# Kernel optimization log

Hardware: AMD Instinct MI355X
Metric: run time of the kernel (lower is better)

The kernel has to match this reference:

```python
import jax, jax.numpy as jnp
import numpy as np

N = 256
DT = 1.0 / 4096.0
BATCH = 256
LENGTH = 4096

def _legt_transition(n):
    # HiPPO-LegT continuous-time transition (Gu et al.)
    Q = np.arange(n, dtype=np.float64)
    R = (2.0 * Q + 1.0) ** 0.5
    j, i = np.meshgrid(Q, Q)
    A = R[:, None] * np.where(i < j, (-1.0) ** (i - j), 1.0) * R[None, :]
    B = R[:, None]
    return -A, B

def _bilinear(A, B, dt):
    # scipy cont2discrete(method='bilinear'), alpha=0.5
    n = A.shape[0]
    ima = np.eye(n) - 0.5 * dt * A
    Ad = np.linalg.solve(ima, np.eye(n) + 0.5 * dt * A)
    Bd = np.linalg.solve(ima, dt * B)
    return Ad, Bd

def setup_inputs() -> dict:
    key = jax.random.key(0)
    Ac, Bc = _legt_transition(N)
    evals = (2.0 * np.arange(N, dtype=np.float64) + 1.0) ** 0.5
    C = evals @ Ac                        # (N,) readout from continuous A
    D = np.sum(evals * Bc.squeeze(-1))    # scalar
    scale = 1.0 / (1.0 - 0.5 * D * DT)
    C_discr = (scale * 0.5 * DT * C).astype(np.float32)          # (N,)
    D_discr = np.array([scale * (1.0 + 0.5 * DT * D)], np.float32)  # (1,)
    Ad, Bd = _bilinear(Ac, Bc, DT)
    inputs = jax.random.normal(key, (BATCH, LENGTH), dtype=jnp.float32)
    return {
        "inputs": inputs,
        "A": jnp.asarray(Ad, dtype=jnp.float32),
        "B": jnp.asarray(Bd.squeeze(-1), dtype=jnp.float32),
        "C_discr": jnp.asarray(C_discr),
        "D_discr": jnp.asarray(D_discr),
    }

def reference(inputs, A, B, C_discr, D_discr):
    # inputs: (batch, length). teacher_ratio=1.0 -> fully teacher-forced LTI scan:
    #   c_t = A c_{t-1} + B * u_t ;  pred_t = fac_t * (c_t @ C) + D * u_t
    # where fac_0 = 1 and fac_t = 2 for t > 0 (as in the torch loop).
    batch, length = inputs.shape
    c0 = jnp.zeros((batch, A.shape[0]), dtype=inputs.dtype)
    facs = jnp.where(jnp.arange(length) == 0, 1.0, 2.0).astype(inputs.dtype)

    def step(c, xs):
        x_t, fac = xs                                   # x_t: (batch,)
        c = c @ A.T + B[None, :] * x_t[:, None]         # (batch, N); F.linear(c, A)
        pred = fac * (c @ C_discr) + D_discr[0] * x_t   # (batch,)
        return c, pred

    _, preds = jax.lax.scan(step, c0, (inputs.T, facs))  # preds: (length, batch)
    return preds.T  # (batch, length)
```

## Files before the change

### kernel.cpp

```cpp
#include <hip/hip_runtime.h>


#define LENGTH 4096

#define WS_P2    0
#define WS_P4    65536
#define WS_P8    131072
#define WS_P16   196608
#define WS_P32   262144
#define WS_P64T  327680
#define WS_P128T 393216
#define WS_W     458752
#define WS_V     475136
#define WS_XH    491520
#define WS_XL    1015808
#define WS_AH    1540096
#define WS_AL    1605632

typedef __attribute__((ext_vector_type(8))) short bf16x8;
typedef __attribute__((ext_vector_type(4))) float f32x4;
#define MFMA(a, b, c) __builtin_amdgcn_mfma_f32_16x16x32_bf16(a, b, c, 0, 0, 0)

__device__ inline unsigned short f2bf(float f) {
    unsigned int u = __float_as_uint(f);
    return (unsigned short)((u + 0x7FFFu + ((u >> 16) & 1u)) >> 16);
}
__device__ inline void split2(float f, short& h, short& l) {
    unsigned short hu = f2bf(f);
    float fh = __uint_as_float((unsigned int)hu << 16);
    h = (short)hu;
    l = (short)f2bf(f - fh);
}

__device__ __forceinline__ void mm_body(const float* __restrict__ X,
                                        const float* __restrict__ Y,
                                        float* __restrict__ Z,
                                        int row, int t, bool trans, float* red) {
    const int j = t & 255, p = t >> 8;
    const float* xr = X + row * 256 + 64 * p;
    const float* yc = Y + (64 * p) * 256 + j;
    float a0 = 0.f, a1 = 0.f, a2 = 0.f, a3 = 0.f;
#pragma unroll
    for (int l = 0; l < 64; l += 4) {
        a0 = fmaf(xr[l + 0], yc[(l + 0) * 256], a0);
        a1 = fmaf(xr[l + 1], yc[(l + 1) * 256], a1);
        a2 = fmaf(xr[l + 2], yc[(l + 2) * 256], a2);
        a3 = fmaf(xr[l + 3], yc[(l + 3) * 256], a3);
    }
    float s = (a0 + a1) + (a2 + a3);
    if (p) red[(p - 1) * 256 + j] = s;
    __syncthreads();
    if (!p) {
        float z = s + red[j] + red[256 + j] + red[512 + j];
        if (trans) Z[j * 256 + row] = z;
        else       Z[row * 256 + j] = z;
    }
}

__global__ __launch_bounds__(1024) void fused0(const float* __restrict__ A,
                                               const float* __restrict__ x,
                                               float* __restrict__ P2,
                                               short* __restrict__ XH,
                                               short* __restrict__ XL) {
    __shared__ float red[3 * 256];
    const int t = threadIdx.x;
    if (blockIdx.x < 256) {
        mm_body(A, A, P2, blockIdx.x, t, false, red);
        return;
    }
    const int wv = t >> 6, lane = t & 63;
    const int pj = (blockIdx.x - 256) * 16 + wv;
    const int c = pj >> 4, blk = pj & 15;
    const int b = blk * 16 + (lane & 15);
    const int s0 = c * 32 + 8 * (lane >> 4);
    const float4 v0 = reinterpret_cast<const float4*>(&x[b * LENGTH + s0])[0];
    const float4 v1 = reinterpret_cast<const float4*>(&x[b * LENGTH + s0])[1];
    const float f[8] = {v0.x, v0.y, v0.z, v0.w, v1.x, v1.y, v1.z, v1.w};
    bf16x8 hv, lv;
#pragma unroll
    for (int e = 0; e < 8; ++e) {
        short h, l;
        split2(f[e], h, l);
        hv[e] = h; lv[e] = l;
    }
    const int off = (pj * 64 + lane) * 8;
    *reinterpret_cast<bf16x8*>(XH + off) = hv;
    *reinterpret_cast<bf16x8*>(XL + off) = lv;
}

__global__ __launch_bounds__(1024) void mmsq(const float* __restrict__ S,
                                             float* __restrict__ D) {
    __shared__ float red[3 * 256];
    mm_body(S, S, D, blockIdx.x, threadIdx.x, false, red);
}
__global__ __launch_bounds__(1024) void mmsqT(const float* __restrict__ S,
                                              float* __restrict__ D) {
    __shared__ float red[3 * 256];
    mm_body(S, S, D, blockIdx.x, threadIdx.x, true, red);
}

__global__ __launch_bounds__(1024) void p128w(const float* __restrict__ P64T,
                                              float* __restrict__ P128T,
                                              const float* __restrict__ A,
                                              const float* __restrict__ C,
                                              const float* __restrict__ P16,
                                              const float* __restrict__ P32,
                                              float* __restrict__ W) {
    __shared__ float red[3 * 256];
    __shared__ float cur[256];
    __shared__ float red4[4][256];
    const int t = threadIdx.x;
    if (blockIdx.x < 256) {
        mm_body(P64T, P64T, P128T, blockIdx.x, t, false, red);
        return;
    }
    const int c = blockIdx.x - 256;
    const int j = t & 255, p = t >> 8;
    float areg[64];
#pragma unroll
    for (int ii = 0; ii < 64; ++ii) areg[ii] = A[(64 * p + ii) * 256 + j];

    if (c == 0) {
        if (t < 256) cur[t] = C[t];
        __syncthreads();
    } else {
        const float* M1 = (c == 2) ? P32 : P16;
        float s0 = 0.f, s1 = 0.f;
#pragma unroll
        for (int ii = 0; ii < 64; ii += 2) {
            s0 = fmaf(C[64 * p + ii],     M1[(64 * p + ii) * 256 + j],     s0);
            s1 = fmaf(C[64 * p + ii + 1], M1[(64 * p + ii + 1) * 256 + j], s1);
        }
        red4[p][j] = s0 + s1;
        __syncthreads();
        if (!p) cur[j] = red4[0][j] + red4[1][j] + red4[2][j] + red4[3][j];
        __syncthreads();
        if (c == 3) {
            float q0 = 0.f, q1 = 0.f;
#pragma unroll
            for (int ii = 0; ii < 64; ii += 2) {
                q0 = fmaf(cur[64 * p + ii],     P32[(64 * p + ii) * 256 + j],     q0);
                q1 = fmaf(cur[64 * p + ii + 1], P32[(64 * p + ii + 1) * 256 + j], q1);
            }
            red4[p][j] = q0 + q1;
            __syncthreads();
            if (!p) cur[j] = red4[0][j] + red4[1][j] + red4[2][j] + red4[3][j];
            __syncthreads();
        }
    }
    for (int s_ = 0; s_ < 16; ++s_) {
        if (!p) W[(16 * c + s_) * 256 + j] = cur[j];
        if (s_ == 15) break;
        float s0 = 0.f, s1 = 0.f;
#pragma unroll
        for (int m = 0; m < 16; ++m) {
            float4 c4 = *reinterpret_cast<const float4*>(&cur[64 * p + 4 * m]);
            s0 = fmaf(c4.x, areg[4 * m + 0], s0);
            s1 = fmaf(c4.y, areg[4 * m + 1], s1);
            s0 = fmaf(c4.z, areg[4 * m + 2], s0);
            s1 = fmaf(c4.w, areg[4 * m + 3], s1);
        }
        red4[p][j] = s0 + s1;
        __syncthreads();
        if (!p) cur[j] = red4[0][j] + red4[1][j] + red4[2][j] + red4[3][j];
        __syncthreads();
    }
}

__global__ __launch_bounds__(1024) void vgen(const float* __restrict__ P64T,
                                             const float* __restrict__ P128T,
                                             const float* __restrict__ B,
                                             float* __restrict__ V) {
    __shared__ float cur[256];
    __shared__ float red4[4][256];
    const int t = threadIdx.x;
    const int i = t & 255, p = t >> 8;
    const int c = blockIdx.x;
    float mreg[64];
#pragma unroll
    for (int jj = 0; jj < 64; ++jj) mreg[jj] = P128T[(64 * p + jj) * 256 + i];

    if (c == 0) {
        if (t < 256) cur[t] = B[t];
        __syncthreads();
    } else {
        float s0 = 0.f, s1 = 0.f;
#pragma unroll
        for (int jj = 0; jj < 64; jj += 2) {
            s0 = fmaf(P64T[(64 * p + jj) * 256 + i],     B[64 * p + jj],     s0);
            s1 = fmaf(P64T[(64 * p + jj + 1) * 256 + i], B[64 * p + jj + 1], s1);
        }
        red4[p][i] = s0 + s1;
        __syncthreads();
        if (!p) cur[i] = red4[0][i] + red4[1][i] + red4[2][i] + red4[3][i];
        __syncthreads();
    }
    for (int s_ = 0; s_ < 32; ++s_) {
        if (!p) V[(2 * s_ + c) * 256 + i] = cur[i];
        if (s_ == 31) break;
        float s0 = 0.f, s1 = 0.f;
#pragma unroll
        for (int m = 0; m < 16; ++m) {
            float4 c4 = *reinterpret_cast<const float4*>(&cur[64 * p + 4 * m]);
            s0 = fmaf(c4.x, mreg[4 * m + 0], s0);
            s1 = fmaf(c4.y, mreg[4 * m + 1], s1);
            s0 = fmaf(c4.z, mreg[4 * m + 2], s0);
            s1 = fmaf(c4.w, mreg[4 * m + 3], s1);
        }
        red4[p][i] = s0 + s1;
        __syncthreads();
        if (!p) cur[i] = red4[0][i] + red4[1][i] + red4[2][i] + red4[3][i];
        __syncthreads();
    }
}

__global__ __launch_bounds__(256) void kfrag(const float* __restrict__ Wm,
                                             const float* __restrict__ Vm,
                                             short* __restrict__ AH,
                                             short* __restrict__ AL) {
    const int bid = blockIdx.x, t = threadIdx.x;
    __shared__ float Wl[64 * 257];
    __shared__ float Vl[3 * 256];
    __shared__ float kl[144];
    for (int r = 0; r < 64; ++r) Wl[r * 257 + t] = Wm[r * 256 + t];
#pragma unroll
    for (int qq = 0; qq < 3; ++qq) {
        const int q = 2 * bid - 1 + qq;
        Vl[qq * 256 + t] = (q >= 0) ? Vm[q * 256 + t] : 0.f;
    }
    __syncthreads();
    if (t < 143) {
        const int tau = 128 * bid - 15 + t;
        float s = 0.f;
        if (tau >= 0) {
            const int r = tau & 63;
            const int qq = (tau >> 6) - (2 * bid - 1);
            const float* wr = &Wl[r * 257];
            const float* vr = &Vl[qq * 256];
            float s0 = 0.f, s1 = 0.f, s2 = 0.f, s3 = 0.f;
#pragma unroll 16
            for (int i = 0; i < 256; i += 4) {
                s0 = fmaf(wr[i + 0], vr[i + 0], s0);
                s1 = fmaf(wr[i + 1], vr[i + 1], s1);
                s2 = fmaf(wr[i + 2], vr[i + 2], s2);
                s3 = fmaf(wr[i + 3], vr[i + 3], s3);
            }
            s = (s0 + s1) + (s2 + s3);
        }
        kl[t] = s;
    }
    __syncthreads();
    const int wv = t >> 6, lane = t & 63;
#pragma unroll
    for (int e2 = 0; e2 < 2; ++e2) {
        const int ep = 2 * wv + e2;
        const int m = 8 * bid + ep;
        bf16x8 hv, lv;
#pragma unroll
        for (int el = 0; el < 8; ++el) {
            const int rel = 16 * ep + (lane & 15) - 8 * (lane >> 4) - el + 15;
            short h, l;
            split2(kl[rel], h, l);
            hv[el] = h; lv[el] = l;
        }
        const int off = (m * 64 + lane) * 8;
        *reinterpret_cast<bf16x8*>(AH + off) = hv;
        *reinterpret_cast<bf16x8*>(AL + off) = lv;
    }
}

#define AHP(M_) (*reinterpret_cast<const bf16x8*>(AH + ((M_) * 64 + lane) * 8))
#define ALP(M_) (*reinterpret_cast<const bf16x8*>(AL + ((M_) * 64 + lane) * 8))
#define XHP(O_) (*reinterpret_cast<const bf16x8*>(XH + (O_)))
#define XLP(O_) (*reinterpret_cast<const bf16x8*>(XL + (O_)))

#define ONER6(AHF, ALF, T, R)                                   \
    acc[T][R][0] = MFMA(AHF, bh0, acc[T][R][0]);                \
    acc[T][R][1] = MFMA(AHF, bh1, acc[T][R][1]);                \
    acc[T][R][0] = MFMA(AHF, bl0, acc[T][R][0]);                \
    acc[T][R][1] = MFMA(AHF, bl1, acc[T][R][1]);                \
    acc[T][R][0] = MFMA(ALF, bh0, acc[T][R][0]);                \
    acc[T][R][1] = MFMA(ALF, bh1, acc[T][R][1]);

#define APPLYT(T)                                               \
    { if (d >= 0)      { ONER6(ah0, al0, T, 0) }                \
      if (d + 16 >= 0) { ONER6(ah1, al1, T, 1) }                \
      if (d + 32 >= 0) { ONER6(ah2, al2, T, 2) }                \
      if (d + 48 >= 0) { ONER6(ah3, al3, T, 3) } }

#define LOADA_FULL(D_)                                          \
    { const int m0_ = ((D_) > 0 ? (D_) : 0) >> 4;               \
      const int m1_ = ((D_) + 16 > 0 ? (D_) + 16 : 0) >> 4;     \
      const int m2_ = ((D_) + 32 > 0 ? (D_) + 32 : 0) >> 4;     \
      const int m3_ = ((D_) + 48 > 0 ? (D_) + 48 : 0) >> 4;     \
      ah0 = AHP(m0_); al0 = ALP(m0_);                           \
      ah1 = AHP(m1_); al1 = ALP(m1_);                           \
      ah2 = AHP(m2_); al2 = ALP(m2_);                           \
      ah3 = AHP(m3_); al3 = ALP(m3_); }

__global__ __launch_bounds__(512) void convm(const short* __restrict__ XH,
                                             const short* __restrict__ XL,
                                             const short* __restrict__ AH,
                                             const short* __restrict__ AL,
                                             const float* __restrict__ x,
                                             const float* __restrict__ Dp,
                                             float* __restrict__ out) {
    const int pr = blockIdx.x & 31;
    const int bt = blockIdx.x >> 5;
    const int tid = threadIdx.x;
    const int w = tid >> 6, lane = tid & 63;
    const int tA64 = pr * 64, tB64 = (63 - pr) * 64;
    const int nA = 2 * pr + 2;
    const int bt2 = bt * 2;
    __shared__ float lds[16 * 64 * 34];

    f32x4 acc[2][4][2];
#pragma unroll
    for (int t_ = 0; t_ < 2; ++t_)
#pragma unroll
        for (int r_ = 0; r_ < 4; ++r_)
#pragma unroll
            for (int c_ = 0; c_ < 2; ++c_) acc[t_][r_][c_] = f32x4{0.f, 0.f, 0.f, 0.f};

    const int lo = (130 * w) >> 3, hi = (130 * (w + 1)) >> 3;

    bf16x8 ah0, ah1, ah2, ah3, al0, al1, al2, al3, bh0, bh1, bl0, bl1;
    int idx = lo;
    int tile = (idx < nA) ? 0 : 1;
    int cc = idx - (tile ? nA : 0);
    int d = (tile ? tB64 : tA64) - 32 * cc;
    LOADA_FULL(d);
    {
        const int xo = ((cc * 16 + bt2) * 64 + lane) * 8;
        bh0 = XHP(xo); bh1 = XHP(xo + 512);
        bl0 = XLP(xo); bl1 = XLP(xo + 512);
    }

    while (true) {
        const int nxt = idx + 1;
        const bool hn = nxt < hi;
        bf16x8 tbh0, tbh1, tbl0, tbl1, tah0, tah1, tal0, tal1;
        int tilen = tile, dn = d;
        bool sw = false;
        if (hn) {
            tilen = (nxt < nA) ? 0 : 1;
            const int ccn = nxt - (tilen ? nA : 0);
            dn = (tilen ? tB64 : tA64) - 32 * ccn;
            sw = (tilen != tile);
            const int xo = ((ccn * 16 + bt2) * 64 + lane) * 8;
            tbh0 = XHP(xo); tbh1 = XHP(xo + 512);
            tbl0 = XLP(xo); tbl1 = XLP(xo + 512);
            if (!sw) {
                const int n0 = (dn > 0 ? dn : 0) >> 4;
                const int n1 = (dn + 16 > 0 ? dn + 16 : 0) >> 4;
                tah0 = AHP(n0); tal0 = ALP(n0);
                tah1 = AHP(n1); tal1 = ALP(n1);
            }
        }
        if (tile == 0) { APPLYT(0) } else { APPLYT(1) }
        if (!hn) break;
        if (!sw) {
            ah3 = ah1; ah2 = ah0; al3 = al1; al2 = al0;
            ah0 = tah0; ah1 = tah1; al0 = tal0; al1 = tal1;
        } else {
            LOADA_FULL(dn);
        }
        bh0 = tbh0; bh1 = tbh1; bl0 = tbl0; bl1 = tbl1;
        tile = tilen; d = dn; idx = nxt;
    }

    const int lq = lane >> 4, lr = lane & 15;
#pragma unroll
    for (int t_ = 0; t_ < 2; ++t_)
#pragma unroll
        for (int r_ = 0; r_ < 4; ++r_)
#pragma unroll
            for (int c_ = 0; c_ < 2; ++c_)
#pragma unroll
                for (int e_ = 0; e_ < 4; ++e_)
                    lds[((w * 2 + t_) * 64 + (r_ * 16 + lq * 4 + e_)) * 34 +
                        (c_ * 16 + lr)] = acc[t_][r_][c_][e_];
    __syncthreads();

    const float D = Dp[0];
    const int b = tid >> 4;
    const int t4 = (tid & 15) * 4;
#pragma unroll
    for (int t_ = 0; t_ < 2; ++t_) {
        const int tbase = t_ ? tB64 : tA64;
        float s0 = 0.f, s1 = 0.f, s2 = 0.f, s3 = 0.f;
#pragma unroll
        for (int w_ = 0; w_ < 8; ++w_) {
            const float* lp = &lds[((w_ * 2 + t_) * 64 + t4) * 34 + b];
            s0 += lp[0]; s1 += lp[34]; s2 += lp[68]; s3 += lp[102];
        }
        const int g = (bt * 32 + b) * LENGTH + tbase + t4;
        const float4 xv = *reinterpret_cast<const float4*>(x + g);
        float4 o;
        o.x = 2.f * s0 + D * xv.x;
        o.y = 2.f * s1 + D * xv.y;
        o.z = 2.f * s2 + D * xv.z;
        o.w = 2.f * s3 + D * xv.w;
        if (tbase == 0 && t4 == 0) o.x -= s0;
        *reinterpret_cast<float4*>(out + g) = o;
    }
}

extern "C" void kernel_launch(void* const* d_in, const int* in_sizes, int n_in,
                              void* d_out, int out_size, void* d_ws, size_t ws_size,
                              hipStream_t stream) {
    const float* x  = (const float*)d_in[0];
    const float* A  = (const float*)d_in[1];
    const float* B  = (const float*)d_in[2];
    const float* C  = (const float*)d_in[3];
    const float* Dp = (const float*)d_in[4];
    float* out = (float*)d_out;
    float* ws  = (float*)d_ws;

    float* P2    = ws + WS_P2;
    float* P4    = ws + WS_P4;
    float* P8    = ws + WS_P8;
    float* P16   = ws + WS_P16;
    float* P32   = ws + WS_P32;
    float* P64T  = ws + WS_P64T;
    float* P128T = ws + WS_P128T;
    float* Wm    = ws + WS_W;
    float* Vm    = ws + WS_V;
    short* XHs   = (short*)(ws + WS_XH);
    short* XLs   = (short*)(ws + WS_XL);
    short* AHs   = (short*)(ws + WS_AH);
    short* ALs   = (short*)(ws + WS_AL);

    fused0<<<384, 1024, 0, stream>>>(A, x, P2, XHs, XLs);
    mmsq<<<256, 1024, 0, stream>>>(P2, P4);
    mmsq<<<256, 1024, 0, stream>>>(P4, P8);
    mmsq<<<256, 1024, 0, stream>>>(P8, P16);
    mmsq<<<256, 1024, 0, stream>>>(P16, P32);
    mmsqT<<<256, 1024, 0, stream>>>(P32, P64T);
    p128w<<<260, 1024, 0, stream>>>(P64T, P128T, A, C, P16, P32, Wm);
    vgen<<<2, 1024, 0, stream>>>(P64T, P128T, B, Vm);
    kfrag<<<32, 256, 0, stream>>>(Wm, Vm, AHs, ALs);
    convm<<<256, 512, 0, stream>>>(XHs, XLs, AHs, ALs, x, Dp, out);
}
```

Baseline: 126.4 us.

## Rebalance precompute kernels and double-buffer fragment loads in convolution kernel

Moves the W-vector generation earlier so it runs alongside the P64 squaring instead of the P128 squaring, and reorders fused0's block roles. kfrag now uses 512 threads, with each wave producing one fragment, so the kernel-fragment generation is spread across more parallelism. convm replaces its contiguous per-wave chunk walk, which shifted A fragments between tiles, with a strided (stride 8) two-frag double-buffered loop that fully reloads A and X fragments each iteration. This aims to overlap loads with MFMA work and to shorten the serial precompute chain, at the cost of more global loads per step and higher register pressure.

After: 120.5 us. 1.05x faster.

```diff
diff --git a/kernel.cpp b/kernel.cpp
--- a/kernel.cpp
+++ b/kernel.cpp
@@ -64,12 +64,12 @@
                                                short* __restrict__ XL) {
     __shared__ float red[3 * 256];
     const int t = threadIdx.x;
-    if (blockIdx.x < 256) {
-        mm_body(A, A, P2, blockIdx.x, t, false, red);
+    if (blockIdx.x >= 128) {
+        mm_body(A, A, P2, blockIdx.x - 128, t, false, red);
         return;
     }
     const int wv = t >> 6, lane = t & 63;
-    const int pj = (blockIdx.x - 256) * 16 + wv;
+    const int pj = blockIdx.x * 16 + wv;
     const int c = pj >> 4, blk = pj & 15;
     const int b = blk * 16 + (lane & 15);
     const int s0 = c * 32 + 8 * (lane >> 4);
@@ -93,28 +93,38 @@
     __shared__ float red[3 * 256];
     mm_body(S, S, D, blockIdx.x, threadIdx.x, false, red);
 }
-__global__ __launch_bounds__(1024) void mmsqT(const float* __restrict__ S,
-                                              float* __restrict__ D) {
-    __shared__ float red[3 * 256];
-    mm_body(S, S, D, blockIdx.x, threadIdx.x, true, red);
-}
-
-__global__ __launch_bounds__(1024) void p128w(const float* __restrict__ P64T,
-                                              float* __restrict__ P128T,
-                                              const float* __restrict__ A,
-                                              const float* __restrict__ C,
-                                              const float* __restrict__ P16,
-                                              const float* __restrict__ P32,
-                                              float* __restrict__ W) {
+
+__device__ __forceinline__ void rv_mm(const float* __restrict__ v,
+                                      const float* __restrict__ M,
+                                      float* curl, float (*red4)[256],
+                                      int j, int p) {
+    float s0 = 0.f, s1 = 0.f;
+#pragma unroll
+    for (int ii = 0; ii < 64; ii += 2) {
+        s0 = fmaf(v[64 * p + ii],     M[(64 * p + ii) * 256 + j],     s0);
+        s1 = fmaf(v[64 * p + ii + 1], M[(64 * p + ii + 1) * 256 + j], s1);
+    }
+    red4[p][j] = s0 + s1;
+    __syncthreads();
+    if (!p) curl[j] = red4[0][j] + red4[1][j] + red4[2][j] + red4[3][j];
+    __syncthreads();
+}
+
+__global__ __launch_bounds__(1024) void p64w(const float* __restrict__ P32,
+                                             float* __restrict__ P64T,
+                                             const float* __restrict__ A,
+                                             const float* __restrict__ C,
+                                             const float* __restrict__ P16,
+                                             float* __restrict__ W) {
     __shared__ float red[3 * 256];
     __shared__ float cur[256];
     __shared__ float red4[4][256];
     const int t = threadIdx.x;
-    if (blockIdx.x < 256) {
-        mm_body(P64T, P64T, P128T, blockIdx.x, t, false, red);
+    if (blockIdx.x >= 4) {
+        mm_body(P32, P32, P64T, blockIdx.x - 4, t, true, red);
         return;
     }
-    const int c = blockIdx.x - 256;
+    const int c = blockIdx.x;
     const int j = t & 255, p = t >> 8;
     float areg[64];
 #pragma unroll
@@ -124,29 +134,8 @@
         if (t < 256) cur[t] = C[t];
         __syncthreads();
     } else {
-        const float* M1 = (c == 2) ? P32 : P16;
-        float s0 = 0.f, s1 = 0.f;
-#pragma unroll
-        for (int ii = 0; ii < 64; ii += 2) {
-            s0 = fmaf(C[64 * p + ii],     M1[(64 * p + ii) * 256 + j],     s0);
-            s1 = fmaf(C[64 * p + ii + 1], M1[(64 * p + ii + 1) * 256 + j], s1);
-        }
-        red4[p][j] = s0 + s1;
-        __syncthreads();
-        if (!p) cur[j] = red4[0][j] + red4[1][j] + red4[2][j] + red4[3][j];
-        __syncthreads();
-        if (c == 3) {
-            float q0 = 0.f, q1 = 0.f;
-#pragma unroll
-            for (int ii = 0; ii < 64; ii += 2) {
-                q0 = fmaf(cur[64 * p + ii],     P32[(64 * p + ii) * 256 + j],     q0);
-                q1 = fmaf(cur[64 * p + ii + 1], P32[(64 * p + ii + 1) * 256 + j], q1);
-            }
-            red4[p][j] = q0 + q1;
-            __syncthreads();
-            if (!p) cur[j] = red4[0][j] + red4[1][j] + red4[2][j] + red4[3][j];
-            __syncthreads();
-        }
+        rv_mm(C, (c == 2) ? P32 : P16, cur, red4, j, p);
+        if (c == 3) rv_mm(cur, P32, cur, red4, j, p);
     }
     for (int s_ = 0; s_ < 16; ++s_) {
         if (!p) W[(16 * c + s_) * 256 + j] = cur[j];
@@ -214,23 +203,23 @@
     }
 }
 
-__global__ __launch_bounds__(256) void kfrag(const float* __restrict__ Wm,
+__global__ __launch_bounds__(512) void kfrag(const float* __restrict__ Wm,
                                              const float* __restrict__ Vm,
                                              short* __restrict__ AH,
                                              short* __restrict__ AL) {
     const int bid = blockIdx.x, t = threadIdx.x;
     __shared__ float Wl[64 * 257];
-    __shared__ float Vl[3 * 256];
-    __shared__ float kl[144];
-    for (int r = 0; r < 64; ++r) Wl[r * 257 + t] = Wm[r * 256 + t];
-#pragma unroll
-    for (int qq = 0; qq < 3; ++qq) {
-        const int q = 2 * bid - 1 + qq;
-        Vl[qq * 256 + t] = (q >= 0) ? Vm[q * 256 + t] : 0.f;
-    }
-    __syncthreads();
-    if (t < 143) {
-        const int tau = 128 * bid - 15 + t;
+    __shared__ float Vl[768];
+    __shared__ float kl[160];
+    for (int u = t; u < 16384; u += 512)
+        Wl[(u >> 8) * 257 + (u & 255)] = Wm[u];
+    for (int u = t; u < 768; u += 512) {
+        const int q = 2 * bid - 1 + (u >> 8);
+        Vl[u] = (q >= 0) ? Vm[q * 256 + (u & 255)] : 0.f;
+    }
+    __syncthreads();
+    if (t < 159) {
+        const int tau = 128 * bid - 31 + t;
         float s = 0.f;
         if (tau >= 0) {
             const int r = tau & 63;
@@ -238,12 +227,12 @@
             const float* wr = &Wl[r * 257];
             const float* vr = &Vl[qq * 256];
             float s0 = 0.f, s1 = 0.f, s2 = 0.f, s3 = 0.f;
-#pragma unroll 16
-            for (int i = 0; i < 256; i += 4) {
-                s0 = fmaf(wr[i + 0], vr[i + 0], s0);
-                s1 = fmaf(wr[i + 1], vr[i + 1], s1);
-                s2 = fmaf(wr[i + 2], vr[i + 2], s2);
-                s3 = fmaf(wr[i + 3], vr[i + 3], s3);
+#pragma unroll 8
+            for (int i2 = 0; i2 < 256; i2 += 4) {
+                s0 = fmaf(wr[i2 + 0], vr[i2 + 0], s0);
+                s1 = fmaf(wr[i2 + 1], vr[i2 + 1], s1);
+                s2 = fmaf(wr[i2 + 2], vr[i2 + 2], s2);
+                s3 = fmaf(wr[i2 + 3], vr[i2 + 3], s3);
             }
             s = (s0 + s1) + (s2 + s3);
         }
@@ -251,52 +240,70 @@
     }
     __syncthreads();
     const int wv = t >> 6, lane = t & 63;
-#pragma unroll
-    for (int e2 = 0; e2 < 2; ++e2) {
-        const int ep = 2 * wv + e2;
-        const int m = 8 * bid + ep;
-        bf16x8 hv, lv;
-#pragma unroll
-        for (int el = 0; el < 8; ++el) {
-            const int rel = 16 * ep + (lane & 15) - 8 * (lane >> 4) - el + 15;
-            short h, l;
-            split2(kl[rel], h, l);
-            hv[el] = h; lv[el] = l;
-        }
-        const int off = (m * 64 + lane) * 8;
-        *reinterpret_cast<bf16x8*>(AH + off) = hv;
-        *reinterpret_cast<bf16x8*>(AL + off) = lv;
-    }
-}
-
-#define AHP(M_) (*reinterpret_cast<const bf16x8*>(AH + ((M_) * 64 + lane) * 8))
-#define ALP(M_) (*reinterpret_cast<const bf16x8*>(AL + ((M_) * 64 + lane) * 8))
-#define XHP(O_) (*reinterpret_cast<const bf16x8*>(XH + (O_)))
-#define XLP(O_) (*reinterpret_cast<const bf16x8*>(XL + (O_)))
-
-#define ONER6(AHF, ALF, T, R)                                   \
-    acc[T][R][0] = MFMA(AHF, bh0, acc[T][R][0]);                \
-    acc[T][R][1] = MFMA(AHF, bh1, acc[T][R][1]);                \
-    acc[T][R][0] = MFMA(AHF, bl0, acc[T][R][0]);                \
-    acc[T][R][1] = MFMA(AHF, bl1, acc[T][R][1]);                \
-    acc[T][R][0] = MFMA(ALF, bh0, acc[T][R][0]);                \
-    acc[T][R][1] = MFMA(ALF, bh1, acc[T][R][1]);
-
-#define APPLYT(T)                                               \
-    { if (d >= 0)      { ONER6(ah0, al0, T, 0) }                \
-      if (d + 16 >= 0) { ONER6(ah1, al1, T, 1) }                \
-      if (d + 32 >= 0) { ONER6(ah2, al2, T, 2) }                \
-      if (d + 48 >= 0) { ONER6(ah3, al3, T, 3) } }
-
-#define LOADA_FULL(D_)                                          \
-    { const int m0_ = ((D_) > 0 ? (D_) : 0) >> 4;               \
-      const int m1_ = ((D_) + 16 > 0 ? (D_) + 16 : 0) >> 4;     \
-      const int m2_ = ((D_) + 32 > 0 ? (D_) + 32 : 0) >> 4;     \
-      const int m3_ = ((D_) + 48 > 0 ? (D_) + 48 : 0) >> 4;     \
-      ah0 = AHP(m0_); al0 = ALP(m0_);                           \
-      ah1 = AHP(m1_); al1 = ALP(m1_);                           \
-      ah2 = AHP(m2_); al2 = ALP(m2_);                           \
-      ah3 = AHP(m3_); al3 = ALP(m3_); }
+    const int m = 8 * bid + wv;
+    bf16x8 hv, lv;
+#pragma unroll
+    for (int el = 0; el < 8; ++el) {
+        const int rel = 16 * wv + (lane & 15) - 8 * (lane >> 4) - el + 31;
+        short h_, l_;
+        split2(kl[rel], h_, l_);
+        hv[el] = h_; lv[el] = l_;
+    }
+    const int off = (m * 64 + lane) * 8;
+    *reinterpret_cast<bf16x8*>(AH + off) = hv;
+    *reinterpret_cast<bf16x8*>(AL + off) = lv;
+}
+
+struct Frag {
+    bf16x8 bh0, bh1, bl0, bl1;
+    bf16x8 ah0, ah1, ah2, ah3, al0, al1, al2, al3;
+    int d0, tile;
+};
+
+#define LOADF(F, IDX_) do {                                                    \
+        const int i_ = (IDX_);                                                 \
+        const int tl_ = (i_ < nA) ? 0 : 1;                                     \
+        const int cc_ = i_ - (tl_ ? nA : 0);                                   \
+        const int xo_ = ((cc_ * 16 + bt2) * 64 + lane) * 8;                    \
+        F.bh0 = *reinterpret_cast<const bf16x8*>(XH + xo_);                    \
+        F.bh1 = *reinterpret_cast<const bf16x8*>(XH + xo_ + 512);              \
+        F.bl0 = *reinterpret_cast<const bf16x8*>(XL + xo_);                    \
+        F.bl1 = *reinterpret_cast<const bf16x8*>(XL + xo_ + 512);              \
+        const int d_ = (tl_ ? tB64 : tA64) - cc_ * 32;                         \
+        F.d0 = d_; F.tile = tl_;                                               \
+        const int m0_ = (d_ > 0 ? d_ : 0) >> 4;                                \
+        const int m1_ = (d_ + 16 > 0 ? d_ + 16 : 0) >> 4;                      \
+        const int m2_ = (d_ + 32 > 0 ? d_ + 32 : 0) >> 4;                      \
+        const int m3_ = (d_ + 48 > 0 ? d_ + 48 : 0) >> 4;                      \
+        F.ah0 = *reinterpret_cast<const bf16x8*>(AH + (m0_ * 64 + lane) * 8);  \
+        F.al0 = *reinterpret_cast<const bf16x8*>(AL + (m0_ * 64 + lane) * 8);  \
+        F.ah1 = *reinterpret_cast<const bf16x8*>(AH + (m1_ * 64 + lane) * 8);  \
+        F.al1 = *reinterpret_cast<const bf16x8*>(AL + (m1_ * 64 + lane) * 8);  \
+        F.ah2 = *reinterpret_cast<const bf16x8*>(AH + (m2_ * 64 + lane) * 8);  \
+        F.al2 = *reinterpret_cast<const bf16x8*>(AL + (m2_ * 64 + lane) * 8);  \
+        F.ah3 = *reinterpret_cast<const bf16x8*>(AH + (m3_ * 64 + lane) * 8);  \
+        F.al3 = *reinterpret_cast<const bf16x8*>(AL + (m3_ * 64 + lane) * 8);  \
+    } while (0)
+
+#define ONER(F, T, R, AHF, ALF)                                                \
+        if (F.d0 + 16 * R >= 0) {                                              \
+            acc[T][R][0] = MFMA(F.AHF, F.bh0, acc[T][R][0]);                   \
+            acc[T][R][1] = MFMA(F.AHF, F.bh1, acc[T][R][1]);                   \
+            acc[T][R][0] = MFMA(F.AHF, F.bl0, acc[T][R][0]);                   \
+            acc[T][R][1] = MFMA(F.AHF, F.bl1, acc[T][R][1]);                   \
+            acc[T][R][0] = MFMA(F.ALF, F.bh0, acc[T][R][0]);                   \
+            acc[T][R][1] = MFMA(F.ALF, F.bh1, acc[T][R][1]);                   \
+        }
+
+#define APPLY(F) do {                                                          \
+        if (F.tile == 0) {                                                     \
+            ONER(F, 0, 0, ah0, al0) ONER(F, 0, 1, ah1, al1)                    \
+            ONER(F, 0, 2, ah2, al2) ONER(F, 0, 3, ah3, al3)                    \
+        } else {                                                               \
+            ONER(F, 1, 0, ah0, al0) ONER(F, 1, 1, ah1, al1)                    \
+            ONER(F, 1, 2, ah2, al2) ONER(F, 1, 3, ah3, al3)                    \
+        }                                                                      \
+    } while (0)
 
 __global__ __launch_bounds__(512) void convm(const short* __restrict__ XH,
                                              const short* __restrict__ XL,
@@ -312,6 +319,7 @@
     const int tA64 = pr * 64, tB64 = (63 - pr) * 64;
     const int nA = 2 * pr + 2;
     const int bt2 = bt * 2;
+
     __shared__ float lds[16 * 64 * 34];
 
     f32x4 acc[2][4][2];
@@ -322,51 +330,21 @@
 #pragma unroll
             for (int c_ = 0; c_ < 2; ++c_) acc[t_][r_][c_] = f32x4{0.f, 0.f, 0.f, 0.f};
 
-    const int lo = (130 * w) >> 3, hi = (130 * (w + 1)) >> 3;
-
-    bf16x8 ah0, ah1, ah2, ah3, al0, al1, al2, al3, bh0, bh1, bl0, bl1;
-    int idx = lo;
-    int tile = (idx < nA) ? 0 : 1;
-    int cc = idx - (tile ? nA : 0);
-    int d = (tile ? tB64 : tA64) - 32 * cc;
-    LOADA_FULL(d);
-    {
-        const int xo = ((cc * 16 + bt2) * 64 + lane) * 8;
-        bh0 = XHP(xo); bh1 = XHP(xo + 512);
-        bl0 = XLP(xo); bl1 = XLP(xo + 512);
-    }
-
+    Frag f0, f1;
+    LOADF(f0, w);
+    int idx = w;
     while (true) {
-        const int nxt = idx + 1;
-        const bool hn = nxt < hi;
-        bf16x8 tbh0, tbh1, tbl0, tbl1, tah0, tah1, tal0, tal1;
-        int tilen = tile, dn = d;
-        bool sw = false;
-        if (hn) {
-            tilen = (nxt < nA) ? 0 : 1;
-            const int ccn = nxt - (tilen ? nA : 0);
-            dn = (tilen ? tB64 : tA64) - 32 * ccn;
-            sw = (tilen != tile);
-            const int xo = ((ccn * 16 + bt2) * 64 + lane) * 8;
-            tbh0 = XHP(xo); tbh1 = XHP(xo + 512);
-            tbl0 = XLP(xo); tbl1 = XLP(xo + 512);
-            if (!sw) {
-                const int n0 = (dn > 0 ? dn : 0) >> 4;
-                const int n1 = (dn + 16 > 0 ? dn + 16 : 0) >> 4;
-                tah0 = AHP(n0); tal0 = ALP(n0);
-                tah1 = AHP(n1); tal1 = ALP(n1);
-            }
-        }
-        if (tile == 0) { APPLYT(0) } else { APPLYT(1) }
-        if (!hn) break;
-        if (!sw) {
-            ah3 = ah1; ah2 = ah0; al3 = al1; al2 = al0;
-            ah0 = tah0; ah1 = tah1; al0 = tal0; al1 = tal1;
-        } else {
-            LOADA_FULL(dn);
-        }
-        bh0 = tbh0; bh1 = tbh1; bl0 = tbl0; bl1 = tbl1;
-        tile = tilen; d = dn; idx = nxt;
+        const int n1 = idx + 8;
+        const bool h1 = n1 < 130;
+        if (h1) LOADF(f1, n1);
+        APPLY(f0);
+        if (!h1) break;
+        const int n2 = n1 + 8;
+        const bool h2 = n2 < 130;
+        if (h2) LOADF(f0, n2);
+        APPLY(f1);
+        if (!h2) break;
+        idx = n2;
     }
 
     const int lq = lane >> 4, lr = lane & 15;
@@ -436,9 +414,9 @@
     mmsq<<<256, 1024, 0, stream>>>(P4, P8);
     mmsq<<<256, 1024, 0, stream>>>(P8, P16);
     mmsq<<<256, 1024, 0, stream>>>(P16, P32);
-    mmsqT<<<256, 1024, 0, stream>>>(P32, P64T);
-    p128w<<<260, 1024, 0, stream>>>(P64T, P128T, A, C, P16, P32, Wm);
+    p64w<<<260, 1024, 0, stream>>>(P32, P64T, A, C, P16, Wm);
+    mmsq<<<256, 1024, 0, stream>>>(P64T, P128T);
     vgen<<<2, 1024, 0, stream>>>(P64T, P128T, B, Vm);
-    kfrag<<<32, 256, 0, stream>>>(Wm, Vm, AHs, ALs);
+    kfrag<<<32, 512, 0, stream>>>(Wm, Vm, AHs, ALs);
     convm<<<256, 512, 0, stream>>>(XHs, XLs, AHs, ALs, x, Dp, out);
 }
```
